# Kernel tuning notes

Hardware: AMD Instinct MI355X
Metric: run time of the kernel (lower is better)

## Reference

```python
import jax, jax.numpy as jnp
from jax import lax
import numpy as np

B, SQ, SK, H, NH, KS = 2, 2048, 2048, 1024, 16, 3
D = H // NH  # depth per head = 64


def setup_inputs() -> dict:
    key = jax.random.key(0)
    ks = jax.random.split(key, 10)
    s = 0.02
    return {
        "query_input": jax.random.normal(ks[0], (B, SQ, H), jnp.float32),
        "source_input": jax.random.normal(ks[1], (B, SK, H), jnp.float32),
        "mask": jnp.zeros((B, 1, 1, SK), jnp.float32),
        "Wq": jax.random.normal(ks[2], (KS, H, H), jnp.float32) * s,
        "bq": jnp.zeros((H,), jnp.float32),
        "Wk": jax.random.normal(ks[3], (KS, H, H), jnp.float32) * s,
        "bk": jnp.zeros((H,), jnp.float32),
        "Wv": jax.random.normal(ks[4], (KS, H, H), jnp.float32) * s,
        "bv": jnp.zeros((H,), jnp.float32),
        "Wo": jax.random.normal(ks[5], (H, H), jnp.float32) * s,
        "bo": jnp.zeros((H,), jnp.float32),
    }


def _conv1d_same(x, W, b):
    # x: [B, S, H], W: [KS, H_in, H_out] -> 'same' padded 1D conv
    y = lax.conv_general_dilated(x, W, window_strides=(1,), padding="SAME",
                                 dimension_numbers=("NWC", "WIO", "NWC"))
    return y + b


def _split_heads(x):
    # [B, S, H] -> [B, NH, S, D]
    b, s, _ = x.shape
    return x.reshape(b, s, NH, D).transpose(0, 2, 1, 3)


def reference(query_input, source_input, mask, Wq, bq, Wk, bk, Wv, bv, Wo, bo):
    q = _split_heads(_conv1d_same(query_input, Wq, bq)) * (D ** -0.5)
    k = _split_heads(_conv1d_same(source_input, Wk, bk))
    v = _split_heads(_conv1d_same(source_input, Wv, bv))
    logits = jnp.einsum("bhqd,bhkd->bhqk", q, k) + mask * (-1e9)
    weights = jax.nn.softmax(logits, axis=-1)  # dropout omitted (eval mode)
    attn = jnp.einsum("bhqk,bhkd->bhqd", weights, v)
    attn = attn.transpose(0, 2, 1, 3).reshape(q.shape[0], -1, H)
    return attn @ Wo + bo
```

## Files before the change

kernel.cpp:

```cpp
#include <hip/hip_runtime.h>
#include <stdint.h>

#define B_   2
#define S_   2048
#define H_   1024
#define NH_  16
#define D_   64
#define KC_  3072

typedef __attribute__((ext_vector_type(8))) short  short8;
typedef __attribute__((ext_vector_type(4))) float  floatx4;

typedef __attribute__((address_space(1))) const void gas_void;
typedef __attribute__((address_space(3))) void       las_void;

__device__ __forceinline__ void gld16(const void* g, void* l) {
    __builtin_amdgcn_global_load_lds((gas_void*)g, (las_void*)l, 16, 0, 0);
}

__device__ __forceinline__ unsigned short f2bf(float f) {
    union { float f; unsigned u; } v; v.f = f;
    unsigned r = v.u + 0x7fffu + ((v.u >> 16) & 1u);
    return (unsigned short)(r >> 16);
}

__global__ __launch_bounds__(256) void k_pad_convert(const float* __restrict__ src,
                                                     unsigned short* __restrict__ dst) {
    int gid = blockIdx.x * 256 + threadIdx.x;
    int vid = gid * 4;
    if (vid >= B_ * 2050 * 1024) return;
    int row = vid >> 10;
    int b   = (row >= 2050) ? 1 : 0;
    int r   = row - b * 2050;
    int h   = vid & 1023;
    unsigned short o0 = 0, o1 = 0, o2 = 0, o3 = 0;
    if (r != 0 && r != 2049) {
        const float4 f = *(const float4*)(src + ((b * 2048 + r - 1) << 10) + h);
        o0 = f2bf(f.x); o1 = f2bf(f.y); o2 = f2bf(f.z); o3 = f2bf(f.w);
    }
    ushort4 o; o.x = o0; o.y = o1; o.z = o2; o.w = o3;
    *(ushort4*)(dst + vid) = o;
}

__global__ void k_transpose_bf16(const float* __restrict__ src,
                                 unsigned short* __restrict__ dst, int R, int C) {
    __shared__ float t[32][33];
    int c0 = blockIdx.x * 32, r0 = blockIdx.y * 32;
    int tx = threadIdx.x, ty = threadIdx.y;
#pragma unroll
    for (int k = 0; k < 4; ++k)
        t[ty + k * 8][tx] = src[(long)(r0 + ty + k * 8) * C + c0 + tx];
    __syncthreads();
#pragma unroll
    for (int k = 0; k < 4; ++k)
        dst[(long)(c0 + ty + k * 8) * R + r0 + tx] = f2bf(t[tx][ty + k * 8]);
}

__global__ __launch_bounds__(256) void k_conv_gemm(
    const unsigned short* __restrict__ xq, const unsigned short* __restrict__ xs,
    const unsigned short* __restrict__ Wqt, const unsigned short* __restrict__ Wkt,
    const unsigned short* __restrict__ Wvt,
    const float* __restrict__ bq, const float* __restrict__ bk, const float* __restrict__ bv,
    unsigned short* __restrict__ Qo, unsigned short* __restrict__ Ko,
    unsigned short* __restrict__ Vo) {
    int z = blockIdx.z;
    const unsigned short* X = (z == 0) ? xq : xs;
    const unsigned short* W = (z == 0) ? Wqt : (z == 1 ? Wkt : Wvt);
    const float* bias = (z == 0) ? bq : (z == 1 ? bk : bv);

    __shared__ unsigned short Al[2][128 * 64];
    __shared__ unsigned short Bl[2][128 * 64];

    int n0 = blockIdx.x * 128, m0 = blockIdx.y * 128;
    int b = m0 >> 11;
    int tid = threadIdx.x, lane = tid & 63, w = tid >> 6;
    int quad = lane >> 4, l15 = lane & 15;
    int wm = w >> 1, wn = w & 1;

    floatx4 acc[4][4];
#pragma unroll
    for (int i = 0; i < 4; ++i)
#pragma unroll
        for (int j = 0; j < 4; ++j) acc[i][j] = (floatx4){0.f, 0.f, 0.f, 0.f};

    int arow0 = (m0 + 2 * b) * 1024;

    int eoff[4], aoff[4], boff[4];
#pragma unroll
    for (int it = 0; it < 4; ++it) {
        int e  = (it * 256 + tid) * 8;
        int rl = e >> 6;
        int cp = (e >> 3) & 7;
        int c  = cp ^ (rl & 7);
        eoff[it] = e;
        aoff[it] = arow0 + rl * 1024 + c * 8;
        boff[it] = (n0 + rl) * KC_ + c * 8;
    }

    auto stage = [&](int buf, int k0) {
#pragma unroll
        for (int it = 0; it < 4; ++it) {
            gld16(X + aoff[it] + k0, (char*)Al[buf] + eoff[it] * 2);
            gld16(W + boff[it] + k0, (char*)Bl[buf] + eoff[it] * 2);
        }
    };
    auto compute = [&](int buf) {
#pragma unroll
        for (int kk = 0; kk < 2; ++kk) {
            short8 af[4], bf[4];
#pragma unroll
            for (int i = 0; i < 4; ++i) {
                int m  = wm * 64 + i * 16 + l15;
                int cp = (kk * 4 + quad) ^ (m & 7);
                af[i]  = *(const short8*)(Al[buf] + m * 64 + cp * 8);
            }
#pragma unroll
            for (int j = 0; j < 4; ++j) {
                int n  = wn * 64 + j * 16 + l15;
                int cp = (kk * 4 + quad) ^ (n & 7);
                bf[j]  = *(const short8*)(Bl[buf] + n * 64 + cp * 8);
            }
#pragma unroll
            for (int i = 0; i < 4; ++i)
#pragma unroll
                for (int j = 0; j < 4; ++j)
                    acc[i][j] = __builtin_amdgcn_mfma_f32_16x16x32_bf16(af[i], bf[j], acc[i][j], 0, 0, 0);
        }
    };

    stage(0, 0);
    __syncthreads();
    for (int kt = 0; kt < 48; kt += 2) {
        if (kt + 1 < 48) stage(1, (kt + 1) * 64);
        compute(0);
        __syncthreads();
        if (kt + 2 < 48) stage(0, (kt + 2) * 64);
        compute(1);
        __syncthreads();
    }

#pragma unroll
    for (int j = 0; j < 4; ++j) {
        int n = n0 + wn * 64 + j * 16 + l15;
        float bb = bias[n];
        int nh = n >> 6, d = n & 63;
#pragma unroll
        for (int i = 0; i < 4; ++i) {
            int srow = (m0 & 2047) + wm * 64 + i * 16 + quad * 4;
#pragma unroll
            for (int r = 0; r < 4; ++r) {
                float v = acc[i][j][r] + bb;
                int s = srow + r;
                if (z == 0)
                    Qo[((b * NH_ + nh) * 2048 + s) * 64 + d] = f2bf(v * 0.125f);
                else if (z == 1)
                    Ko[((b * NH_ + nh) * 2048 + s) * 64 + d] = f2bf(v);
                else
                    Vo[((b * NH_ + nh) * 64 + d) * 2048 + s] = f2bf(v);
            }
        }
    }
}

__global__ __launch_bounds__(256) void k_flash(
    const unsigned short* __restrict__ Q, const unsigned short* __restrict__ K,
    const unsigned short* __restrict__ Vt, const float* __restrict__ mask,
    unsigned short* __restrict__ Ao) {
    __shared__ unsigned short Ul[128 * 136];
    __shared__ unsigned short Vl[64 * 128];

    int tid = threadIdx.x, w = tid >> 6, lane = tid & 63;
    int quad = lane >> 4, l15 = lane & 15;
    int bh = blockIdx.y;
    int b = bh >> 4, nh = bh & 15;
    int q0 = blockIdx.x * 128, wq = w * 32;

    short8 qf[2][2];
#pragma unroll
    for (int i = 0; i < 2; ++i)
#pragma unroll
        for (int kk = 0; kk < 2; ++kk)
            qf[i][kk] = *(const short8*)(Q + ((bh * 2048 + q0 + wq + i * 16 + l15) << 6) + kk * 32 + quad * 8);

    floatx4 oacc[2][4];
    float rsum[2][4];
#pragma unroll
    for (int i = 0; i < 2; ++i) {
#pragma unroll
        for (int j = 0; j < 4; ++j) oacc[i][j] = (floatx4){0.f, 0.f, 0.f, 0.f};
#pragma unroll
        for (int r = 0; r < 4; ++r) rsum[i][r] = 0.f;
    }
    const float* maskb = mask + b * S_;

    for (int kt = 0; kt < 16; ++kt) {
        int k0 = kt * 128;
#pragma unroll
        for (int it = 0; it < 4; ++it) {
            int e  = (it * 256 + tid) * 8;
            int kl = e >> 6;
            int c  = ((e >> 3) & 7) ^ (kl & 7);
            gld16(K + (bh * 2048 + k0 + kl) * 64 + c * 8, (char*)Ul + e * 2);
            int dl = e >> 7;
            int cp = (e >> 3) & 15;
            int c2 = (cp & 8) | ((cp ^ dl) & 7);
            gld16(Vt + (bh * 64 + dl) * 2048 + k0 + c2 * 8, (char*)Vl + e * 2);
        }
        __syncthreads();

        floatx4 sacc[2][8];
#pragma unroll
        for (int i = 0; i < 2; ++i)
#pragma unroll
            for (int j = 0; j < 8; ++j) sacc[i][j] = (floatx4){0.f, 0.f, 0.f, 0.f};
#pragma unroll
        for (int j = 0; j < 8; ++j) {
            int kl = j * 16 + l15;
            int cp0 = (0 * 4 + quad) ^ (kl & 7);
            short8 bf0 = *(const short8*)(Ul + kl * 64 + cp0 * 8);
            int cp1 = (1 * 4 + quad) ^ (kl & 7);
            short8 bf1 = *(const short8*)(Ul + kl * 64 + cp1 * 8);
#pragma unroll
            for (int i = 0; i < 2; ++i) {
                sacc[i][j] = __builtin_amdgcn_mfma_f32_16x16x32_bf16(qf[i][0], bf0, sacc[i][j], 0, 0, 0);
                sacc[i][j] = __builtin_amdgcn_mfma_f32_16x16x32_bf16(qf[i][1], bf1, sacc[i][j], 0, 0, 0);
            }
        }
        __syncthreads();

#pragma unroll
        for (int j = 0; j < 8; ++j) {
            float mv = maskb[k0 + j * 16 + l15] * (-1e9f);
#pragma unroll
            for (int i = 0; i < 2; ++i) {
                int row = wq + i * 16 + quad * 4;
#pragma unroll
                for (int r = 0; r < 4; ++r) {
                    float p = __expf(sacc[i][j][r] + mv);
                    rsum[i][r] += p;
                    Ul[(row + r) * 136 + j * 16 + l15] = f2bf(p);
                }
            }
        }

#pragma unroll
        for (int kk = 0; kk < 4; ++kk) {
            short8 af[2], bv4[4];
#pragma unroll
            for (int i = 0; i < 2; ++i)
                af[i] = *(const short8*)(Ul + (wq + i * 16 + l15) * 136 + kk * 32 + quad * 8);
#pragma unroll
            for (int j2 = 0; j2 < 4; ++j2) {
                int dl = j2 * 16 + l15;
                int c  = kk * 4 + quad;
                int cp = (c & 8) | ((c ^ dl) & 7);
                bv4[j2] = *(const short8*)(Vl + dl * 128 + cp * 8);
            }
#pragma unroll
            for (int i = 0; i < 2; ++i)
#pragma unroll
                for (int j2 = 0; j2 < 4; ++j2)
                    oacc[i][j2] = __builtin_amdgcn_mfma_f32_16x16x32_bf16(af[i], bv4[j2], oacc[i][j2], 0, 0, 0);
        }
        __syncthreads();
    }

#pragma unroll
    for (int i = 0; i < 2; ++i)
#pragma unroll
        for (int r = 0; r < 4; ++r) {
            float v = rsum[i][r];
            v += __shfl_xor(v, 1); v += __shfl_xor(v, 2);
            v += __shfl_xor(v, 4); v += __shfl_xor(v, 8);
            rsum[i][r] = 1.0f / v;
        }

#pragma unroll
    for (int i = 0; i < 2; ++i)
#pragma unroll
        for (int j2 = 0; j2 < 4; ++j2)
#pragma unroll
            for (int r = 0; r < 4; ++r) {
                int qrow = q0 + wq + i * 16 + quad * 4 + r;
                int hcol = nh * 64 + j2 * 16 + l15;
                Ao[(b * 2048 + qrow) * 1024 + hcol] = f2bf(oacc[i][j2][r] * rsum[i][r]);
            }
}

__global__ __launch_bounds__(256) void k_proj_gemm(
    const unsigned short* __restrict__ A, const unsigned short* __restrict__ Wt,
    const float* __restrict__ bo, float* __restrict__ out) {
    __shared__ unsigned short Al[2][128 * 64];
    __shared__ unsigned short Bl[2][128 * 64];

    int n0 = blockIdx.x * 128, m0 = blockIdx.y * 128;
    int tid = threadIdx.x, lane = tid & 63, w = tid >> 6;
    int quad = lane >> 4, l15 = lane & 15;
    int wm = w >> 1, wn = w & 1;

    floatx4 acc[4][4];
#pragma unroll
    for (int i = 0; i < 4; ++i)
#pragma unroll
        for (int j = 0; j < 4; ++j) acc[i][j] = (floatx4){0.f, 0.f, 0.f, 0.f};

    int eoff[4], aoff[4], boff[4];
#pragma unroll
    for (int it = 0; it < 4; ++it) {
        int e  = (it * 256 + tid) * 8;
        int rl = e >> 6;
        int c  = ((e >> 3) & 7) ^ (rl & 7);
        eoff[it] = e;
        aoff[it] = (m0 + rl) * 1024 + c * 8;
        boff[it] = (n0 + rl) * 1024 + c * 8;
    }

    auto stage = [&](int buf, int k0) {
#pragma unroll
        for (int it = 0; it < 4; ++it) {
            gld16(A + aoff[it] + k0, (char*)Al[buf] + eoff[it] * 2);
            gld16(Wt + boff[it] + k0, (char*)Bl[buf] + eoff[it] * 2);
        }
    };
    auto compute = [&](int buf) {
#pragma unroll
        for (int kk = 0; kk < 2; ++kk) {
            short8 af[4], bf[4];
#pragma unroll
            for (int i = 0; i < 4; ++i) {
                int m  = wm * 64 + i * 16 + l15;
                int cp = (kk * 4 + quad) ^ (m & 7);
                af[i]  = *(const short8*)(Al[buf] + m * 64 + cp * 8);
            }
#pragma unroll
            for (int j = 0; j < 4; ++j) {
                int n  = wn * 64 + j * 16 + l15;
                int cp = (kk * 4 + quad) ^ (n & 7);
                bf[j]  = *(const short8*)(Bl[buf] + n * 64 + cp * 8);
            }
#pragma unroll
            for (int i = 0; i < 4; ++i)
#pragma unroll
                for (int j = 0; j < 4; ++j)
                    acc[i][j] = __builtin_amdgcn_mfma_f32_16x16x32_bf16(af[i], bf[j], acc[i][j], 0, 0, 0);
        }
    };

    stage(0, 0);
    __syncthreads();
    for (int kt = 0; kt < 16; kt += 2) {
        if (kt + 1 < 16) stage(1, (kt + 1) * 64);
        compute(0);
        __syncthreads();
        if (kt + 2 < 16) stage(0, (kt + 2) * 64);
        compute(1);
        __syncthreads();
    }

#pragma unroll
    for (int j = 0; j < 4; ++j) {
        int n = n0 + wn * 64 + j * 16 + l15;
        float bb = bo[n];
#pragma unroll
        for (int i = 0; i < 4; ++i) {
            int m = m0 + wm * 64 + i * 16 + quad * 4;
#pragma unroll
            for (int r = 0; r < 4; ++r)
                out[(m + r) * 1024 + n] = acc[i][j][r] + bb;
        }
    }
}

extern "C" void kernel_launch(void* const* d_in, const int* in_sizes, int n_in,
                              void* d_out, int out_size, void* d_ws, size_t ws_size,
                              hipStream_t stream) {
    (void)in_sizes; (void)n_in; (void)out_size; (void)ws_size;
    const float* q_in = (const float*)d_in[0];
    const float* s_in = (const float*)d_in[1];
    const float* mask = (const float*)d_in[2];
    const float* Wq   = (const float*)d_in[3];
    const float* bq   = (const float*)d_in[4];
    const float* Wk   = (const float*)d_in[5];
    const float* bk   = (const float*)d_in[6];
    const float* Wv   = (const float*)d_in[7];
    const float* bv   = (const float*)d_in[8];
    const float* Wo   = (const float*)d_in[9];
    const float* bo   = (const float*)d_in[10];
    float* out = (float*)d_out;

    char* ws = (char*)d_ws;
    size_t off = 0;
    auto alloc = [&](size_t bytes) {
        char* p = ws + off;
        off += (bytes + 255) & ~(size_t)255;
        return p;
    };
    unsigned short* xqp = (unsigned short*)alloc((size_t)B_ * 2050 * 1024 * 2);
    unsigned short* xsp = (unsigned short*)alloc((size_t)B_ * 2050 * 1024 * 2);
    unsigned short* Wqt = (unsigned short*)alloc((size_t)KC_ * H_ * 2);
    unsigned short* Wkt = (unsigned short*)alloc((size_t)KC_ * H_ * 2);
    unsigned short* Wvt = (unsigned short*)alloc((size_t)KC_ * H_ * 2);
    unsigned short* Wot = (unsigned short*)alloc((size_t)H_ * H_ * 2);
    unsigned short* Qb  = (unsigned short*)alloc((size_t)B_ * NH_ * S_ * D_ * 2);
    unsigned short* Kb  = (unsigned short*)alloc((size_t)B_ * NH_ * S_ * D_ * 2);
    unsigned short* Vtb = (unsigned short*)alloc((size_t)B_ * NH_ * S_ * D_ * 2);
    unsigned short* Ab  = (unsigned short*)alloc((size_t)B_ * S_ * H_ * 2);

    k_pad_convert<<<4100, 256, 0, stream>>>(q_in, xqp);
    k_pad_convert<<<4100, 256, 0, stream>>>(s_in, xsp);
    k_transpose_bf16<<<dim3(32, 96), dim3(32, 8), 0, stream>>>(Wq, Wqt, KC_, H_);
    k_transpose_bf16<<<dim3(32, 96), dim3(32, 8), 0, stream>>>(Wk, Wkt, KC_, H_);
    k_transpose_bf16<<<dim3(32, 96), dim3(32, 8), 0, stream>>>(Wv, Wvt, KC_, H_);
    k_transpose_bf16<<<dim3(32, 32), dim3(32, 8), 0, stream>>>(Wo, Wot, H_, H_);
    k_conv_gemm<<<dim3(8, 32, 3), 256, 0, stream>>>(xqp, xsp, Wqt, Wkt, Wvt,
                                                    bq, bk, bv, Qb, Kb, Vtb);
    k_flash<<<dim3(16, 32), 256, 0, stream>>>(Qb, Kb, Vtb, mask, Ab);
    k_proj_gemm<<<dim3(8, 32), 256, 0, stream>>>(Ab, Wot, bo, out);
}
```

Baseline: 361.3 us.

## Reuse one shared input tile across the three conv taps in the QKV GEMM

The conv-as-GEMM kernel now loads a 130-row activation tile once per 64-channel chunk and reads it at row offsets 0, 1 and 2 for the three kernel taps, loading all three weight slices together. This cuts global reads of the activation by about three times and reduces the K-loop count. It removes the double-buffered prefetch, so loads are no longer overlapped with MFMA work. It also raises shared-memory use, which may lower occupancy.

```diff
diff --git a/kernel.cpp b/kernel.cpp
--- a/kernel.cpp
+++ b/kernel.cpp
@@ -68,8 +68,8 @@
     const unsigned short* W = (z == 0) ? Wqt : (z == 1 ? Wkt : Wvt);
     const float* bias = (z == 0) ? bq : (z == 1 ? bk : bv);
 
-    __shared__ unsigned short Al[2][128 * 64];
-    __shared__ unsigned short Bl[2][128 * 64];
+    __shared__ unsigned short Al[132 * 64];
+    __shared__ unsigned short Bl[3 * 128 * 64];
 
     int n0 = blockIdx.x * 128, m0 = blockIdx.y * 128;
     int b = m0 >> 11;
@@ -83,59 +83,76 @@
 #pragma unroll
         for (int j = 0; j < 4; ++j) acc[i][j] = (floatx4){0.f, 0.f, 0.f, 0.f};
 
-    int arow0 = (m0 + 2 * b) * 1024;
-
-    int eoff[4], aoff[4], boff[4];
+    const unsigned short* Xbase = X + (m0 + 2 * b) * 1024;
+
+    int eaA[4], oaA[4];
 #pragma unroll
     for (int it = 0; it < 4; ++it) {
         int e  = (it * 256 + tid) * 8;
-        int rl = e >> 6;
+        int r  = e >> 6;
         int cp = (e >> 3) & 7;
+        int c  = cp ^ (r & 7);
+        eaA[it] = e;
+        oaA[it] = r * 1024 + c * 8;
+    }
+    int eaX = 0, oaX = 0;
+    if (tid < 16) {
+        int e  = (1024 + tid) * 8;
+        int r  = 128 + (tid >> 3);
+        int cp = tid & 7;
+        int c  = cp ^ (r & 7);
+        eaX = e;
+        oaX = r * 1024 + c * 8;
+    }
+    int eaB[12], oaB[12];
+#pragma unroll
+    for (int it = 0; it < 12; ++it) {
+        int e  = (it * 256 + tid) * 8;
+        int t  = e >> 13;
+        int er = e & 8191;
+        int rl = er >> 6;
+        int cp = (er >> 3) & 7;
         int c  = cp ^ (rl & 7);
-        eoff[it] = e;
-        aoff[it] = arow0 + rl * 1024 + c * 8;
-        boff[it] = (n0 + rl) * KC_ + c * 8;
-    }
-
-    auto stage = [&](int buf, int k0) {
-#pragma unroll
-        for (int it = 0; it < 4; ++it) {
-            gld16(X + aoff[it] + k0, (char*)Al[buf] + eoff[it] * 2);
-            gld16(W + boff[it] + k0, (char*)Bl[buf] + eoff[it] * 2);
-        }
-    };
-    auto compute = [&](int buf) {
-#pragma unroll
-        for (int kk = 0; kk < 2; ++kk) {
-            short8 af[4], bf[4];
-#pragma unroll
-            for (int i = 0; i < 4; ++i) {
-                int m  = wm * 64 + i * 16 + l15;
-                int cp = (kk * 4 + quad) ^ (m & 7);
-                af[i]  = *(const short8*)(Al[buf] + m * 64 + cp * 8);
-            }
-#pragma unroll
-            for (int j = 0; j < 4; ++j) {
-                int n  = wn * 64 + j * 16 + l15;
-                int cp = (kk * 4 + quad) ^ (n & 7);
-                bf[j]  = *(const short8*)(Bl[buf] + n * 64 + cp * 8);
-            }
-#pragma unroll
-            for (int i = 0; i < 4; ++i)
-#pragma unroll
-                for (int j = 0; j < 4; ++j)
-                    acc[i][j] = __builtin_amdgcn_mfma_f32_16x16x32_bf16(af[i], bf[j], acc[i][j], 0, 0, 0);
-        }
-    };
-
-    stage(0, 0);
-    __syncthreads();
-    for (int kt = 0; kt < 48; kt += 2) {
-        if (kt + 1 < 48) stage(1, (kt + 1) * 64);
-        compute(0);
-        __syncthreads();
-        if (kt + 2 < 48) stage(0, (kt + 2) * 64);
-        compute(1);
+        eaB[it] = e;
+        oaB[it] = (n0 + rl) * KC_ + t * 1024 + c * 8;
+    }
+
+    for (int kt = 0; kt < 16; ++kt) {
+        int k0 = kt * 64;
+#pragma unroll
+        for (int it = 0; it < 4; ++it)
+            gld16(Xbase + oaA[it] + k0, (char*)Al + eaA[it] * 2);
+        if (tid < 16)
+            gld16(Xbase + oaX + k0, (char*)Al + eaX * 2);
+#pragma unroll
+        for (int it = 0; it < 12; ++it)
+            gld16(W + oaB[it] + k0, (char*)Bl + eaB[it] * 2);
+        __syncthreads();
+
+#pragma unroll
+        for (int t = 0; t < 3; ++t) {
+#pragma unroll
+            for (int kk = 0; kk < 2; ++kk) {
+                short8 af[4], bf[4];
+#pragma unroll
+                for (int i = 0; i < 4; ++i) {
+                    int r  = wm * 64 + i * 16 + l15 + t;
+                    int cp = (kk * 4 + quad) ^ (r & 7);
+                    af[i]  = *(const short8*)(Al + r * 64 + cp * 8);
+                }
+#pragma unroll
+                for (int j = 0; j < 4; ++j) {
+                    int n  = wn * 64 + j * 16 + l15;
+                    int cp = (kk * 4 + quad) ^ (n & 7);
+                    bf[j]  = *(const short8*)(Bl + t * 8192 + n * 64 + cp * 8);
+                }
+#pragma unroll
+                for (int i = 0; i < 4; ++i)
+#pragma unroll
+                    for (int j = 0; j < 4; ++j)
+                        acc[i][j] = __builtin_amdgcn_mfma_f32_16x16x32_bf16(af[i], bf[j], acc[i][j], 0, 0, 0);
+            }
+        }
         __syncthreads();
     }
 
```

Result: faster. 316.9 us (-12.3%).
